# Optimization experiments

Hardware: AMD Instinct MI355X
Metric: run time of the kernel (lower is better)

Reference implementation:

```python
import jax, jax.numpy as jnp
import numpy as np

B, S, HID = 2, 2048, 2048
NH, HD = 16, 128            # num heads, head dim (HID = NH*HD)
ROT = 64                    # rotary_dim
MASK_VALUE = -10000.0


def _rotate_every_two(x):
    # x: [..., d] with d even; interleaved (-x2, x1)
    x1 = x[..., ::2]
    x2 = x[..., 1::2]
    return jnp.stack((-x2, x1), axis=-1).reshape(x.shape)


def _fixed_sincos(seq_len, dim):
    inv_freq = 1.0 / (10000.0 ** (jnp.arange(0, dim, 2, dtype=jnp.float32) / dim))
    t = jnp.arange(seq_len, dtype=jnp.float32)
    ang = t[:, None] * inv_freq[None, :]          # [S, dim/2]
    return jnp.sin(ang), jnp.cos(ang)


def _apply_rope(x, sin, cos):
    # x: [B, S, H, rot]; sin/cos: [S, rot/2] -> repeat_interleave(2) -> [S, rot]
    sin = jnp.repeat(sin, 2, axis=-1)[None, :, None, :]
    cos = jnp.repeat(cos, 2, axis=-1)[None, :, None, :]
    return x * cos + _rotate_every_two(x) * sin


def setup_inputs() -> dict:
    key = jax.random.key(0)
    ks = jax.random.split(key, 7)
    w_scale = 1.0 / np.sqrt(HID)
    return {
        "hidden_states": jax.random.normal(ks[0], (B, S, HID), dtype=jnp.float32),
        "attention_mask": jnp.zeros((B, 1, 1, S), dtype=jnp.float32),
        "Wq": jax.random.normal(ks[1], (HID, HID), dtype=jnp.float32) * w_scale,
        "bq": jnp.zeros((HID,), dtype=jnp.float32),
        "Wk": jax.random.normal(ks[2], (HID, HID), dtype=jnp.float32) * w_scale,
        "bk": jnp.zeros((HID,), dtype=jnp.float32),
        "Wv": jax.random.normal(ks[3], (HID, HID), dtype=jnp.float32) * w_scale,
        "bv": jnp.zeros((HID,), dtype=jnp.float32),
    }


def reference(hidden_states, attention_mask, Wq, bq, Wk, bk, Wv, bv):
    # QKV projections (torch Linear: x @ W.T + b)
    q = (hidden_states @ Wq.T + bq).reshape(B, S, NH, HD)
    k = (hidden_states @ Wk.T + bk).reshape(B, S, NH, HD)
    v = (hidden_states @ Wv.T + bv).reshape(B, S, NH, HD)

    # Inline rotary on first ROT dims of q/k
    sin, cos = _fixed_sincos(S, ROT)
    q = jnp.concatenate([_apply_rope(q[..., :ROT], sin, cos), q[..., ROT:]], axis=-1)
    k = jnp.concatenate([_apply_rope(k[..., :ROT], sin, cos), k[..., ROT:]], axis=-1)

    # Scores [B, H, S, S]
    scores = jnp.einsum('bqhd,bkhd->bhqk', q, k) / np.sqrt(HD)

    # Causal mask + additive attention mask
    causal = jnp.tril(jnp.ones((S, S), dtype=bool))[None, None]
    scores = jnp.where(causal, scores, jnp.asarray(MASK_VALUE, scores.dtype))
    scores = scores + attention_mask

    probs = jax.nn.softmax(scores, axis=-1)
    ctx = jnp.einsum('bhqk,bkhd->bqhd', probs, v)
    return ctx.reshape(B, S, HID)
```

## Files before the change

### kernel.cpp

```cpp
#include <hip/hip_runtime.h>

typedef unsigned short bhalf;
typedef __attribute__((ext_vector_type(4))) float    f32x4;
typedef __attribute__((ext_vector_type(8))) short    s16x8;
typedef __attribute__((ext_vector_type(4))) float    floatx4;
typedef __attribute__((ext_vector_type(4))) unsigned short u16x4;

#define B_  2
#define S_  2048
#define HID_ 2048
#define NH_ 16
#define HD_ 128
#define M_  (B_*S_)
#define MASKV (-10000.0f)

__device__ __forceinline__ bhalf f32_to_bf16(float f) {
    union { float f; unsigned int u; } v; v.f = f;
    unsigned int r = v.u + 0x7FFFu + ((v.u >> 16) & 1u);
    return (bhalf)(r >> 16);
}
__device__ __forceinline__ bhalf f32_to_bf16_trunc(float f) {
    union { float f; unsigned int u; } v; v.f = f;
    return (bhalf)(v.u >> 16);
}
__device__ __forceinline__ float bf16_to_f32(bhalf h) {
    union { unsigned int u; float f; } v; v.u = ((unsigned int)h) << 16;
    return v.f;
}

__device__ __forceinline__ void gl_lds16(const void* g, void* l) {
    __builtin_amdgcn_global_load_lds(
        (const __attribute__((address_space(1))) void*)g,
        (__attribute__((address_space(3))) void*)l, 16, 0, 0);
}

#define BARRIER() asm volatile("s_barrier" ::: "memory")

__global__ __launch_bounds__(256) void cast_all(const float* __restrict__ hs,
                                                const float* __restrict__ Wq,
                                                const float* __restrict__ Wk,
                                                const float* __restrict__ Wv,
                                                bhalf* __restrict__ dst,
                                                float2* __restrict__ tab) {
    if (blockIdx.x >= 20480) {
        int idx = (blockIdx.x - 20480) * 256 + threadIdx.x;
        int i = idx & 31, s = idx >> 5;
        float inv = expf(-(float)i * 0.2878231366242557f);
        float ang = (float)s * inv;
        tab[idx] = make_float2(sinf(ang), cosf(ang));
        return;
    }
    int idx = blockIdx.x * 256 + threadIdx.x;
    const float* src;
    if (idx < 2097152)      src = hs + (size_t)idx * 4;
    else if (idx < 3145728) src = Wq + (size_t)(idx - 2097152) * 4;
    else if (idx < 4194304) src = Wk + (size_t)(idx - 3145728) * 4;
    else                    src = Wv + (size_t)(idx - 4194304) * 4;
    floatx4 f = *(const floatx4*)src;
    u16x4 o;
    o.x = f32_to_bf16(f.x); o.y = f32_to_bf16(f.y);
    o.z = f32_to_bf16(f.z); o.w = f32_to_bf16(f.w);
    *(u16x4*)(dst + (size_t)idx * 4) = o;
}

__global__ __launch_bounds__(512, 2) void qkv_gemm(const bhalf* __restrict__ A,
                                                   const bhalf* __restrict__ Wb,
                                                   const float* __restrict__ bq,
                                                   const float* __restrict__ bk,
                                                   const float* __restrict__ bv,
                                                   bhalf* __restrict__ Out,
                                                   bhalf* __restrict__ VTo) {
    __shared__ __align__(16) bhalf As[2][16384];
    __shared__ __align__(16) bhalf Bs[2][8192];
    const int tid  = threadIdx.x;
    const int lane = tid & 63, w = tid >> 6;
    const int quad = lane >> 4, l = lane & 15;
    const int wy = w >> 1, wx = w & 1;
    const int m0 = blockIdx.x * 256, n0 = blockIdx.y * 128;
    const int z  = blockIdx.z;
    const bhalf* W    = Wb + (size_t)z * HID_ * HID_;
    const float* bias = (z == 0) ? bq : (z == 1) ? bk : bv;
    bhalf* out        = Out + (size_t)z * M_ * HID_;

    bhalf* AsF = &As[0][0];
    bhalf* BsF = &Bs[0][0];

    const int row_s = tid >> 3;
    const int kg_s  = (tid & 7) ^ (row_s & 7);
    const int w512  = w * 512;

    const bhalf* gA0 = A + (size_t)(m0 +   0 + row_s) * HID_ + kg_s * 8;
    const bhalf* gA1 = A + (size_t)(m0 +  64 + row_s) * HID_ + kg_s * 8;
    const bhalf* gA2 = A + (size_t)(m0 + 128 + row_s) * HID_ + kg_s * 8;
    const bhalf* gA3 = A + (size_t)(m0 + 192 + row_s) * HID_ + kg_s * 8;
    const bhalf* gB0 = W + (size_t)(n0 +   0 + row_s) * HID_ + kg_s * 8;
    const bhalf* gB1 = W + (size_t)(n0 +  64 + row_s) * HID_ + kg_s * 8;

    const int aIdx = (wy * 64 + l) * 64;
    const int bIdx = (wx * 64 + l) * 64;
    const int swz0 = ((0 + quad) ^ (l & 7)) * 8;
    const int swz1 = ((4 + quad) ^ (l & 7)) * 8;

    f32x4 acc[4][4] = {};

#define ADV() do { gA0 += 64; gA1 += 64; gA2 += 64; gA3 += 64;               \
                   gB0 += 64; gB1 += 64; } while (0)

#define KTILE(BUF, ST1, ST2, VM) do {                                        \
    const int CA = (BUF) * 16384, NA = ((BUF) ^ 1) * 16384;                  \
    const int CBB = (BUF) * 8192;                                            \
    s16x8 a_[4][2], b01_[2][2], b23_[2][2];                                  \
              \
    _Pragma("unroll") for (int mt = 0; mt < 4; ++mt) {                       \
        a_[mt][0] = *(const s16x8*)(AsF + CA + aIdx + mt * 1024 + swz0);     \
        a_[mt][1] = *(const s16x8*)(AsF + CA + aIdx + mt * 1024 + swz1); }   \
    _Pragma("unroll") for (int nt = 0; nt < 2; ++nt) {                       \
        b01_[nt][0] = *(const s16x8*)(BsF + CBB + bIdx + nt * 1024 + swz0);  \
        b01_[nt][1] = *(const s16x8*)(BsF + CBB + bIdx + nt * 1024 + swz1); }\
    if (ST1) { gl_lds16(gA2 + 64, AsF + NA + 2 * 4096 + w512);               \
               gl_lds16(gA3 + 64, AsF + NA + 3 * 4096 + w512); }             \
    BARRIER();                                                               \
    __builtin_amdgcn_s_setprio(1);                                           \
    _Pragma("unroll") for (int mt = 0; mt < 2; ++mt)                         \
      _Pragma("unroll") for (int nt = 0; nt < 2; ++nt)                       \
        _Pragma("unroll") for (int ks = 0; ks < 2; ++ks)                     \
          acc[mt][nt] = __builtin_amdgcn_mfma_f32_16x16x32_bf16(             \
              a_[mt][ks], b01_[nt][ks], acc[mt][nt], 0, 0, 0);               \
    __builtin_amdgcn_s_setprio(0);                                           \
    BARRIER();                                                               \
    \
    _Pragma("unroll") for (int nt = 0; nt < 2; ++nt) {                       \
        b23_[nt][0] = *(const s16x8*)(BsF + CBB + bIdx + (nt+2)*1024 + swz0);\
        b23_[nt][1] = *(const s16x8*)(BsF + CBB + bIdx + (nt+2)*1024 + swz1);}\
    if (ST2) { gl_lds16(gA0 + 128, AsF + CA + 0 * 4096 + w512);              \
               gl_lds16(gA1 + 128, AsF + CA + 1 * 4096 + w512); }            \
    BARRIER();                                                               \
    __builtin_amdgcn_s_setprio(1);                                           \
    _Pragma("unroll") for (int mt = 0; mt < 2; ++mt)                         \
      _Pragma("unroll") for (int nt = 0; nt < 2; ++nt)                       \
        _Pragma("unroll") for (int ks = 0; ks < 2; ++ks)                     \
          acc[mt][nt + 2] = __builtin_amdgcn_mfma_f32_16x16x32_bf16(         \
              a_[mt][ks], b23_[nt][ks], acc[mt][nt + 2], 0, 0, 0);           \
    __builtin_amdgcn_s_setprio(0);                                           \
    BARRIER();                                                               \
                  \
    if (ST2) { gl_lds16(gB0 + 128, BsF + CBB + 0 * 4096 + w512);             \
               gl_lds16(gB1 + 128, BsF + CBB + 1 * 4096 + w512); }           \
    BARRIER();                                                               \
    __builtin_amdgcn_s_setprio(1);                                           \
    _Pragma("unroll") for (int mt = 0; mt < 2; ++mt)                         \
      _Pragma("unroll") for (int nt = 0; nt < 2; ++nt)                       \
        _Pragma("unroll") for (int ks = 0; ks < 2; ++ks)                     \
          acc[2 + mt][nt] = __builtin_amdgcn_mfma_f32_16x16x32_bf16(         \
              a_[2 + mt][ks], b01_[nt][ks], acc[2 + mt][nt], 0, 0, 0);       \
    __builtin_amdgcn_s_setprio(0);                                           \
    BARRIER();                                                               \
                           \
    if ((VM) == 4)      asm volatile("s_waitcnt vmcnt(4)" ::: "memory");     \
    else if ((VM) == 0) asm volatile("s_waitcnt vmcnt(0)" ::: "memory");     \
    BARRIER();                                                               \
    __builtin_amdgcn_s_setprio(1);                                           \
    _Pragma("unroll") for (int mt = 0; mt < 2; ++mt)                         \
      _Pragma("unroll") for (int nt = 0; nt < 2; ++nt)                       \
        _Pragma("unroll") for (int ks = 0; ks < 2; ++ks)                     \
          acc[2 + mt][nt + 2] = __builtin_amdgcn_mfma_f32_16x16x32_bf16(     \
              a_[2 + mt][ks], b23_[nt][ks], acc[2 + mt][nt + 2], 0, 0, 0);   \
    __builtin_amdgcn_s_setprio(0);                                           \
    BARRIER();                                                               \
} while (0)

    gl_lds16(gA0, AsF + 0 * 4096 + w512);
    gl_lds16(gA1, AsF + 1 * 4096 + w512);
    gl_lds16(gA2, AsF + 2 * 4096 + w512);
    gl_lds16(gA3, AsF + 3 * 4096 + w512);
    gl_lds16(gB0, BsF + 0 * 4096 + w512);
    gl_lds16(gB1, BsF + 1 * 4096 + w512);
    gl_lds16(gA0 + 64, AsF + 16384 + 0 * 4096 + w512);
    gl_lds16(gA1 + 64, AsF + 16384 + 1 * 4096 + w512);
    gl_lds16(gB0 + 64, BsF + 8192 + 0 * 4096 + w512);
    gl_lds16(gB1 + 64, BsF + 8192 + 1 * 4096 + w512);
    asm volatile("s_waitcnt vmcnt(4)" ::: "memory");
    BARRIER();

    for (int tt = 0; tt < 15; ++tt) {
        KTILE(0, 1, 1, 4); ADV();
        KTILE(1, 1, 1, 4); ADV();
    }
    KTILE(0, 1, 0, 0); ADV();
    KTILE(1, 0, 0, -1);

#undef KTILE
#undef ADV

    if (z == 2) {
#pragma unroll
        for (int mt = 0; mt < 4; ++mt) {
#pragma unroll
            for (int nt = 0; nt < 4; ++nt) {
                int col = n0 + wx * 64 + nt * 16 + l;
                float bv_ = bias[col];
                int row0 = m0 + wy * 64 + mt * 16 + quad * 4;
                int bb = row0 >> 11, s0 = row0 & 2047;
                u16x4 o;
#pragma unroll
                for (int r = 0; r < 4; ++r) o[r] = f32_to_bf16(acc[mt][nt][r] + bv_);
                *(u16x4*)(VTo + ((size_t)(bb * 16) * 128 + col) * S_ + s0) = o;
            }
        }
    } else {
#pragma unroll
        for (int mt = 0; mt < 4; ++mt) {
#pragma unroll
            for (int nt = 0; nt < 4; ++nt) {
                int col = n0 + wx * 64 + nt * 16 + l;
                float bv_ = bias[col];
#pragma unroll
                for (int r = 0; r < 4; ++r) {
                    int row = m0 + wy * 64 + mt * 16 + quad * 4 + r;
                    out[(size_t)row * HID_ + col] = f32_to_bf16(acc[mt][nt][r] + bv_);
                }
            }
        }
    }
}

__global__ __launch_bounds__(256) void rope_apply(bhalf* __restrict__ Qb,
                                                  bhalf* __restrict__ Kb,
                                                  const float2* __restrict__ tab) {
    int flat = blockIdx.x * 256 + threadIdx.x;
    int i = flat & 31;
    int h = (flat >> 5) & 15;
    int s = (flat >> 9) & 2047;
    int b = flat >> 20;
    size_t base = ((size_t)(b * S_ + s)) * HID_ + h * HD_ + 2 * i;
    float2 sc = tab[s * 32 + i];
    float c = sc.y, sn = sc.x;
    {
        unsigned int q = *(const unsigned int*)(Qb + base);
        float x0 = bf16_to_f32((bhalf)(q & 0xffff));
        float x1 = bf16_to_f32((bhalf)(q >> 16));
        unsigned int o = (unsigned int)f32_to_bf16(x0 * c - x1 * sn)
                       | ((unsigned int)f32_to_bf16(x1 * c + x0 * sn) << 16);
        *(unsigned int*)(Qb + base) = o;
    }
    {
        unsigned int k = *(const unsigned int*)(Kb + base);
        float x0 = bf16_to_f32((bhalf)(k & 0xffff));
        float x1 = bf16_to_f32((bhalf)(k >> 16));
        unsigned int o = (unsigned int)f32_to_bf16(x0 * c - x1 * sn)
                       | ((unsigned int)f32_to_bf16(x1 * c + x0 * sn) << 16);
        *(unsigned int*)(Kb + base) = o;
    }
}

__global__ __launch_bounds__(256, 2) void flash_attn(const bhalf* __restrict__ Qb,
                                                     const bhalf* __restrict__ Kb,
                                                     const bhalf* __restrict__ VT,
                                                     const float* __restrict__ amask,
                                                     float* __restrict__ out) {
    __shared__ __align__(16) bhalf Kbuf[2][1024 * 8];
    __shared__ __align__(16) bhalf Vbuf[2][1024 * 8];
    __shared__ __align__(16) bhalf Pbuf[4][1024];
    const int tid = threadIdx.x, lane = tid & 63, w = tid >> 6;
    const int quad = lane >> 4, l = lane & 15;
    const int bh = blockIdx.x, pr = blockIdx.y;
    const int b = bh >> 4, h = bh & 15;
    s16x8 ones;
#pragma unroll
    for (int j = 0; j < 8; ++j) ones[j] = (short)0x3F80;
    const int fpl = ((l >> 2) << 1) | (l & 1);

    for (int pass = 0; pass < 2; ++pass) {
        const int qt = pass ? (31 - pr) : pr;
        const int myrow = qt * 64 + w * 16;
        const int nch = qt + 1;

        s16x8 qf[4];
        {
            const bhalf* Qrow = Qb + (size_t)(b * S_ + myrow + l) * HID_ + h * HD_;
#pragma unroll
            for (int ks = 0; ks < 4; ++ks)
                qf[ks] = *(const s16x8*)(Qrow + ks * 32 + quad * 8);
        }

        float m_run[4] = {-1e30f, -1e30f, -1e30f, -1e30f};
        f32x4 l_acc = {};
        f32x4 acc[8] = {};

        __syncthreads();

#pragma unroll
        for (int j = 0; j < 4; ++j) {
            int slot0 = j * 256 + w * 64;
            int slot  = slot0 + lane;
            {
                int row = slot >> 4, x = slot & 15;
                int g   = (x & 8) | ((x ^ row) & 7);
                gl_lds16(Kb + (size_t)(b * S_ + row) * HID_ + h * HD_ + g * 8,
                         &Kbuf[0][slot0 * 8]);
            }
            {
                int row = slot >> 3, x = slot & 7;
                int g   = (x ^ row) & 7;
                gl_lds16(VT + ((size_t)bh * HD_ + row) * S_ + g * 8,
                         &Vbuf[0][slot0 * 8]);
            }
        }

        for (int kc = 0; kc < nch; ++kc) {
            const int cur = kc & 1, nxt = cur ^ 1;
            const int key0 = kc * 64;
            __syncthreads();

            const bool diag = (kc == qt);

            float am[4];
#pragma unroll
            for (int nt = 0; nt < 4; ++nt) am[nt] = amask[b * S_ + key0 + nt * 16 + l];
            if (kc + 1 < nch) {
                const int key1 = key0 + 64;
#pragma unroll
                for (int j = 0; j < 4; ++j) {
                    int slot0 = j * 256 + w * 64;
                    int slot  = slot0 + lane;
                    {
                        int row = slot >> 4, x = slot & 15;
                        int g   = (x & 8) | ((x ^ row) & 7);
                        gl_lds16(Kb + (size_t)(b * S_ + key1 + row) * HID_ + h * HD_ + g * 8,
                                 &Kbuf[nxt][slot0 * 8]);
                    }
                    {
                        int row = slot >> 3, x = slot & 7;
                        int g   = (x ^ row) & 7;
                        gl_lds16(VT + ((size_t)bh * HD_ + row) * S_ + key1 + g * 8,
                                 &Vbuf[nxt][slot0 * 8]);
                    }
                }
            }

            const bhalf* Kc = &Kbuf[cur][0];
            const bhalf* Vc = &Vbuf[cur][0];
            bhalf* Pw = &Pbuf[w][0];

            f32x4 s[4] = {};
            __builtin_amdgcn_s_setprio(1);
#pragma unroll
            for (int nt = 0; nt < 4; ++nt) {
                int key = nt * 16 + l;
#pragma unroll
                for (int ks = 0; ks < 4; ++ks) {
                    int dg = ks * 4 + quad;
                    int x  = (dg & 8) | ((dg ^ key) & 7);
                    s16x8 kf = *(const s16x8*)(Kc + (key * 16 + x) * 8);
                    s[nt] = __builtin_amdgcn_mfma_f32_16x16x32_bf16(qf[ks], kf, s[nt], 0, 0, 0);
                }
            }
            __builtin_amdgcn_s_setprio(0);

#pragma unroll
            for (int r = 0; r < 4; ++r) {
                const int qrow = myrow + quad * 4 + r;
                float p[4];
#pragma unroll
                for (int nt = 0; nt < 4; ++nt) {
                    float v = s[nt][r] * 0.08838834764831845f;
                    if (diag) { int key = key0 + nt * 16 + l; v = (key > qrow) ? MASKV : v; }
                    p[nt] = v + am[nt];
                }
                float mx = fmaxf(fmaxf(p[0], p[1]), fmaxf(p[2], p[3]));
#pragma unroll
                for (int msk = 1; msk < 16; msk <<= 1) mx = fmaxf(mx, __shfl_xor(mx, msk, 64));
                float m_new = fmaxf(m_run[r], mx);
                float alpha = __expf(m_run[r] - m_new);
                m_run[r] = m_new;
                const int m  = quad * 4 + r;
                const int fm = (quad << 1) | (r & 1);
#pragma unroll
                for (int nt = 0; nt < 4; ++nt) {
                    float e = __expf(p[nt] - m_new);
                    int key = nt * 16 + l;
                    Pw[(m * 8 + ((key >> 3) ^ fm)) * 8 + (key & 7)] = f32_to_bf16_trunc(e);
                }
                l_acc[r] *= alpha;
#pragma unroll
                for (int nt = 0; nt < 8; ++nt) acc[nt][r] *= alpha;
            }
            __builtin_amdgcn_s_setprio(1);
#pragma unroll
            for (int kstep = 0; kstep < 2; ++kstep) {
                int kg = kstep * 4 + quad;
                s16x8 pf = *(const s16x8*)(Pw + (l * 8 + (kg ^ fpl)) * 8);
                l_acc = __builtin_amdgcn_mfma_f32_16x16x32_bf16(pf, ones, l_acc, 0, 0, 0);
#pragma unroll
                for (int nt = 0; nt < 8; ++nt) {
                    int d = nt * 16 + l;
                    int x = (kg ^ d) & 7;
                    s16x8 vf = *(const s16x8*)(Vc + (d * 8 + x) * 8);
                    acc[nt] = __builtin_amdgcn_mfma_f32_16x16x32_bf16(pf, vf, acc[nt], 0, 0, 0);
                }
            }
            __builtin_amdgcn_s_setprio(0);
        }

        float inv[4];
#pragma unroll
        for (int r = 0; r < 4; ++r) inv[r] = 1.f / l_acc[r];
#pragma unroll
        for (int nt = 0; nt < 8; ++nt) {
            int col = h * HD_ + nt * 16 + l;
#pragma unroll
            for (int r = 0; r < 4; ++r)
                out[(size_t)(b * S_ + myrow + quad * 4 + r) * HID_ + col] = acc[nt][r] * inv[r];
        }
    }
}

extern "C" void kernel_launch(void* const* d_in, const int* in_sizes, int n_in,
                              void* d_out, int out_size, void* d_ws, size_t ws_size,
                              hipStream_t stream) {
    const float* hs    = (const float*)d_in[0];
    const float* amask = (const float*)d_in[1];
    const float* Wq    = (const float*)d_in[2];
    const float* bq    = (const float*)d_in[3];
    const float* Wk    = (const float*)d_in[4];
    const float* bk    = (const float*)d_in[5];
    const float* Wv    = (const float*)d_in[6];
    const float* bv    = (const float*)d_in[7];
    float* out = (float*)d_out;

    bhalf* hsb = (bhalf*)d_ws;
    bhalf* wqb = hsb + 8388608;
    bhalf* wkb = wqb + 4194304;
    bhalf* wvb = wkb + 4194304;
    bhalf* Qb  = wvb + 4194304;
    bhalf* Kb  = Qb + 8388608;
    bhalf* VTb = Kb + 8388608;
    float2* tab = (float2*)(VTb + 8388608);

    cast_all<<<20736, 256, 0, stream>>>(hs, Wq, Wk, Wv, hsb, tab);
    qkv_gemm<<<dim3(16, 16, 3), 512, 0, stream>>>(hsb, wqb, bq, bk, bv, Qb, VTb);
    rope_apply<<<8192, 256, 0, stream>>>(Qb, Kb, tab);
    flash_attn<<<dim3(32, 16), 256, 0, stream>>>(Qb, Kb, VTb, amask, out);
}
```

Before: 319.6 us.

## Compute transposed scores to keep P in registers via lane shuffles

Swaps the MFMA operand order so each lane holds scores for a single query row. The softmax reduction then needs two cross-lane shuffles instead of four per row. The probability tile is repacked into the A-operand layout with lane shuffles instead of a round trip through shared memory. The row-sum MFMA against a ones vector is replaced by a scalar running sum. This drops LDS writes and reads and one MFMA per k-step, at the cost of extra shuffles and selects.

Result: no change. 321.8 us (+0.7%).

```diff
diff --git a/kernel.cpp b/kernel.cpp
--- a/kernel.cpp
+++ b/kernel.cpp
@@ -26,6 +26,10 @@
 __device__ __forceinline__ float bf16_to_f32(bhalf h) {
     union { unsigned int u; float f; } v; v.u = ((unsigned int)h) << 16;
     return v.f;
+}
+__device__ __forceinline__ unsigned int bfpack(float a, float b) {
+    return (unsigned int)f32_to_bf16_trunc(a) |
+           ((unsigned int)f32_to_bf16_trunc(b) << 16);
 }
 
 __device__ __forceinline__ void gl_lds16(const void* g, void* l) {
@@ -260,31 +264,29 @@
                                                      float* __restrict__ out) {
     __shared__ __align__(16) bhalf Kbuf[2][1024 * 8];
     __shared__ __align__(16) bhalf Vbuf[2][1024 * 8];
-    __shared__ __align__(16) bhalf Pbuf[4][1024];
     const int tid = threadIdx.x, lane = tid & 63, w = tid >> 6;
     const int quad = lane >> 4, l = lane & 15;
     const int bh = blockIdx.x, pr = blockIdx.y;
     const int b = bh >> 4, h = bh & 15;
-    s16x8 ones;
-#pragma unroll
-    for (int j = 0; j < 8; ++j) ones[j] = (short)0x3F80;
-    const int fpl = ((l >> 2) << 1) | (l & 1);
+    const int qsel = quad >> 1;
+    const int srcA = l + ((quad & 1) << 5);
+    const int srcB = srcA + 16;
 
     for (int pass = 0; pass < 2; ++pass) {
         const int qt = pass ? (31 - pr) : pr;
         const int myrow = qt * 64 + w * 16;
         const int nch = qt + 1;
+        const int qrow = myrow + l;
 
         s16x8 qf[4];
         {
-            const bhalf* Qrow = Qb + (size_t)(b * S_ + myrow + l) * HID_ + h * HD_;
+            const bhalf* Qrow = Qb + (size_t)(b * S_ + qrow) * HID_ + h * HD_;
 #pragma unroll
             for (int ks = 0; ks < 4; ++ks)
                 qf[ks] = *(const s16x8*)(Qrow + ks * 32 + quad * 8);
         }
 
-        float m_run[4] = {-1e30f, -1e30f, -1e30f, -1e30f};
-        f32x4 l_acc = {};
+        float m_run = -1e30f, l_run = 0.f;
         f32x4 acc[8] = {};
 
         __syncthreads();
@@ -314,9 +316,10 @@
 
             const bool diag = (kc == qt);
 
-            float am[4];
-#pragma unroll
-            for (int nt = 0; nt < 4; ++nt) am[nt] = amask[b * S_ + key0 + nt * 16 + l];
+            float4 am4[4];
+#pragma unroll
+            for (int nt = 0; nt < 4; ++nt)
+                am4[nt] = *(const float4*)(amask + b * S_ + key0 + nt * 16 + quad * 4);
             if (kc + 1 < nch) {
                 const int key1 = key0 + 64;
 #pragma unroll
@@ -340,77 +343,115 @@
 
             const bhalf* Kc = &Kbuf[cur][0];
             const bhalf* Vc = &Vbuf[cur][0];
-            bhalf* Pw = &Pbuf[w][0];
 
             f32x4 s[4] = {};
             __builtin_amdgcn_s_setprio(1);
 #pragma unroll
             for (int nt = 0; nt < 4; ++nt) {
-                int key = nt * 16 + l;
+                int row = nt * 16 + l;
 #pragma unroll
                 for (int ks = 0; ks < 4; ++ks) {
                     int dg = ks * 4 + quad;
-                    int x  = (dg & 8) | ((dg ^ key) & 7);
-                    s16x8 kf = *(const s16x8*)(Kc + (key * 16 + x) * 8);
-                    s[nt] = __builtin_amdgcn_mfma_f32_16x16x32_bf16(qf[ks], kf, s[nt], 0, 0, 0);
+                    int x  = (dg & 8) | ((dg ^ row) & 7);
+                    s16x8 kf = *(const s16x8*)(Kc + (row * 16 + x) * 8);
+                    s[nt] = __builtin_amdgcn_mfma_f32_16x16x32_bf16(kf, qf[ks], s[nt], 0, 0, 0);
                 }
             }
             __builtin_amdgcn_s_setprio(0);
 
-#pragma unroll
-            for (int r = 0; r < 4; ++r) {
-                const int qrow = myrow + quad * 4 + r;
-                float p[4];
-#pragma unroll
-                for (int nt = 0; nt < 4; ++nt) {
+            float p[4][4];
+#pragma unroll
+            for (int nt = 0; nt < 4; ++nt) {
+                float amv[4] = {am4[nt].x, am4[nt].y, am4[nt].z, am4[nt].w};
+#pragma unroll
+                for (int r = 0; r < 4; ++r) {
                     float v = s[nt][r] * 0.08838834764831845f;
-                    if (diag) { int key = key0 + nt * 16 + l; v = (key > qrow) ? MASKV : v; }
-                    p[nt] = v + am[nt];
-                }
-                float mx = fmaxf(fmaxf(p[0], p[1]), fmaxf(p[2], p[3]));
-#pragma unroll
-                for (int msk = 1; msk < 16; msk <<= 1) mx = fmaxf(mx, __shfl_xor(mx, msk, 64));
-                float m_new = fmaxf(m_run[r], mx);
-                float alpha = __expf(m_run[r] - m_new);
-                m_run[r] = m_new;
-                const int m  = quad * 4 + r;
-                const int fm = (quad << 1) | (r & 1);
-#pragma unroll
-                for (int nt = 0; nt < 4; ++nt) {
-                    float e = __expf(p[nt] - m_new);
-                    int key = nt * 16 + l;
-                    Pw[(m * 8 + ((key >> 3) ^ fm)) * 8 + (key & 7)] = f32_to_bf16_trunc(e);
-                }
-                l_acc[r] *= alpha;
-#pragma unroll
-                for (int nt = 0; nt < 8; ++nt) acc[nt][r] *= alpha;
-            }
+                    if (diag) {
+                        int key = key0 + nt * 16 + quad * 4 + r;
+                        v = (key > qrow) ? MASKV : v;
+                    }
+                    p[nt][r] = v + amv[r];
+                }
+            }
+            float mx = p[0][0];
+#pragma unroll
+            for (int nt = 0; nt < 4; ++nt)
+#pragma unroll
+                for (int r = 0; r < 4; ++r) mx = fmaxf(mx, p[nt][r]);
+            mx = fmaxf(mx, __shfl_xor(mx, 16, 64));
+            mx = fmaxf(mx, __shfl_xor(mx, 32, 64));
+            float m_new = fmaxf(m_run, mx);
+            float alpha = __expf(m_run - m_new);
+            m_run = m_new;
+            float lsum = 0.f;
+#pragma unroll
+            for (int nt = 0; nt < 4; ++nt)
+#pragma unroll
+                for (int r = 0; r < 4; ++r) {
+                    p[nt][r] = __expf(p[nt][r] - m_new);
+                    lsum += p[nt][r];
+                }
+            lsum += __shfl_xor(lsum, 16, 64);
+            lsum += __shfl_xor(lsum, 32, 64);
+            l_run = l_run * alpha + lsum;
+
+            float alphar[4];
+#pragma unroll
+            for (int r = 0; r < 4; ++r) alphar[r] = __shfl(alpha, quad * 4 + r, 64);
+#pragma unroll
+            for (int nt = 0; nt < 8; ++nt)
+#pragma unroll
+                for (int r = 0; r < 4; ++r) acc[nt][r] *= alphar[r];
+
+            unsigned int plo[4], phi[4];
+#pragma unroll
+            for (int nt = 0; nt < 4; ++nt) {
+                plo[nt] = bfpack(p[nt][0], p[nt][1]);
+                phi[nt] = bfpack(p[nt][2], p[nt][3]);
+            }
+            s16x8 pa[2];
+#pragma unroll
+            for (int ks = 0; ks < 2; ++ks) {
+                unsigned int aL0 = __shfl((int)plo[ks * 2],     srcA, 64);
+                unsigned int aL1 = __shfl((int)plo[ks * 2 + 1], srcA, 64);
+                unsigned int aH0 = __shfl((int)phi[ks * 2],     srcA, 64);
+                unsigned int aH1 = __shfl((int)phi[ks * 2 + 1], srcA, 64);
+                unsigned int bL0 = __shfl((int)plo[ks * 2],     srcB, 64);
+                unsigned int bL1 = __shfl((int)plo[ks * 2 + 1], srcB, 64);
+                unsigned int bH0 = __shfl((int)phi[ks * 2],     srcB, 64);
+                unsigned int bH1 = __shfl((int)phi[ks * 2 + 1], srcB, 64);
+                union { unsigned int u[4]; s16x8 v; } cv;
+                cv.u[0] = qsel ? aL1 : aL0;
+                cv.u[1] = qsel ? aH1 : aH0;
+                cv.u[2] = qsel ? bL1 : bL0;
+                cv.u[3] = qsel ? bH1 : bH0;
+                pa[ks] = cv.v;
+            }
+
             __builtin_amdgcn_s_setprio(1);
 #pragma unroll
-            for (int kstep = 0; kstep < 2; ++kstep) {
-                int kg = kstep * 4 + quad;
-                s16x8 pf = *(const s16x8*)(Pw + (l * 8 + (kg ^ fpl)) * 8);
-                l_acc = __builtin_amdgcn_mfma_f32_16x16x32_bf16(pf, ones, l_acc, 0, 0, 0);
+            for (int ks = 0; ks < 2; ++ks) {
+                int kg = ks * 4 + quad;
 #pragma unroll
                 for (int nt = 0; nt < 8; ++nt) {
                     int d = nt * 16 + l;
                     int x = (kg ^ d) & 7;
                     s16x8 vf = *(const s16x8*)(Vc + (d * 8 + x) * 8);
-                    acc[nt] = __builtin_amdgcn_mfma_f32_16x16x32_bf16(pf, vf, acc[nt], 0, 0, 0);
+                    acc[nt] = __builtin_amdgcn_mfma_f32_16x16x32_bf16(pa[ks], vf, acc[nt], 0, 0, 0);
                 }
             }
             __builtin_amdgcn_s_setprio(0);
         }
 
-        float inv[4];
-#pragma unroll
-        for (int r = 0; r < 4; ++r) inv[r] = 1.f / l_acc[r];
+        float linv[4];
+#pragma unroll
+        for (int r = 0; r < 4; ++r) linv[r] = 1.f / __shfl(l_run, quad * 4 + r, 64);
 #pragma unroll
         for (int nt = 0; nt < 8; ++nt) {
             int col = h * HD_ + nt * 16 + l;
 #pragma unroll
             for (int r = 0; r < 4; ++r)
-                out[(size_t)(b * S_ + myrow + quad * 4 + r) * HID_ + col] = acc[nt][r] * inv[r];
+                out[(size_t)(b * S_ + myrow + quad * 4 + r) * HID_ + col] = acc[nt][r] * linv[r];
         }
     }
 }
```
